# Performance work log

Measured on AMD Instinct MI355X. Metric: run time of the kernel, lower is better.

Reference implementation:

```python
import jax, jax.numpy as jnp
import numpy as np

N = 50000      # nodes
E = 800000     # edges (before self loops)
DIN = 128      # input feature dim
H = 2          # attention heads
C = 64         # per-head hidden channels (hidden_dim)
HC = H * C     # 128, concat output width of each GATv2 layer
DOUT = 4       # NUM_LANES
NEG = 0.2      # GATv2 default negative_slope


def _w(key, fan_in, shape):
    return jax.random.normal(key, shape, dtype=jnp.float32) * (1.0 / np.sqrt(fan_in))


def setup_inputs() -> dict:
    key = jax.random.key(0)
    ks = jax.random.split(key, 32)
    inp = {
        "x": jax.random.normal(ks[0], (N, DIN), dtype=jnp.float32),
        "edge_index": jax.random.randint(ks[1], (2, E), 0, N, dtype=jnp.int64),
    }
    # layer 1: DIN -> H*C
    inp["W1l"] = _w(ks[2], DIN, (DIN, HC)); inp["b1l"] = jnp.zeros((HC,), jnp.float32)
    inp["W1r"] = _w(ks[3], DIN, (DIN, HC)); inp["b1r"] = jnp.zeros((HC,), jnp.float32)
    inp["att1"] = _w(ks[4], C, (H, C));     inp["bias1"] = jnp.zeros((HC,), jnp.float32)
    # layer 2: H*C -> H*C
    inp["W2l"] = _w(ks[5], HC, (HC, HC));   inp["b2l"] = jnp.zeros((HC,), jnp.float32)
    inp["W2r"] = _w(ks[6], HC, (HC, HC));   inp["b2r"] = jnp.zeros((HC,), jnp.float32)
    inp["att2"] = _w(ks[7], C, (H, C));     inp["bias2"] = jnp.zeros((HC,), jnp.float32)
    # layer 3: H*C -> H*C
    inp["W3l"] = _w(ks[8], HC, (HC, HC));   inp["b3l"] = jnp.zeros((HC,), jnp.float32)
    inp["W3r"] = _w(ks[9], HC, (HC, HC));   inp["b3r"] = jnp.zeros((HC,), jnp.float32)
    inp["att3"] = _w(ks[10], C, (H, C));    inp["bias3"] = jnp.zeros((HC,), jnp.float32)
    # output linear
    inp["Wout"] = _w(ks[11], HC, (HC, DOUT)); inp["bout"] = jnp.zeros((DOUT,), jnp.float32)
    return inp


def gat_layer(x, src, dst, Wl, bl, Wr, br, att, bias):
    # GATv2Conv, concat=True, add_self_loops already in src/dst.
    n = x.shape[0]
    h, c = att.shape
    xl = (x @ Wl + bl).reshape(n, h, c)   # source transform
    xr = (x @ Wr + br).reshape(n, h, c)   # target transform
    m = xl[src] + xr[dst]                               # [Etot, H, C]
    e = jnp.sum(jax.nn.leaky_relu(m, NEG) * att, -1)    # [Etot, H]
    emax = jax.ops.segment_max(e, dst, num_segments=n)  # segment softmax over in-edges
    p = jnp.exp(e - emax[dst])
    denom = jax.ops.segment_sum(p, dst, num_segments=n)
    alpha = p / denom[dst]                              # [Etot, H]
    out = jax.ops.segment_sum(alpha[:, :, None] * xl[src], dst, num_segments=n)
    return out.reshape(n, h * c) + bias


def reference(x, edge_index, W1l, b1l, W1r, b1r, att1, bias1,
              W2l, b2l, W2r, b2r, att2, bias2,
              W3l, b3l, W3r, b3r, att3, bias3, Wout, bout):
    n = x.shape[0]
    loop = jnp.arange(n, dtype=edge_index.dtype)
    src = jnp.concatenate([edge_index[0], loop])  # add self loops (PyG default)
    dst = jnp.concatenate([edge_index[1], loop])
    h = jax.nn.relu(gat_layer(x, src, dst, W1l, b1l, W1r, b1r, att1, bias1))
    h = jax.nn.relu(gat_layer(h, src, dst, W2l, b2l, W2r, b2r, att2, bias2))
    h = jax.nn.relu(gat_layer(h, src, dst, W3l, b3l, W3r, b3r, att3, bias3))
    return h @ Wout + bout
```

## Files before the change

### kernel.cpp

```cpp
#include <hip/hip_runtime.h>
#include <math.h>

#define DIN  128
#define HC   128
#define NEG  0.2f

typedef __attribute__((ext_vector_type(4))) float f32x4;
typedef __attribute__((ext_vector_type(8))) _Float16 half8;
typedef __attribute__((ext_vector_type(2))) _Float16 half2v;

__device__ __forceinline__ int colOf(int p) {
    return ((p >> 5) * 2 + (p & 1)) * 16 + ((p & 31) >> 1);
}

template <int CTRL>
__device__ __forceinline__ float dpp_xadd(float x) {
    int r = __builtin_amdgcn_update_dpp(0, __float_as_int(x), CTRL, 0xF, 0xF, true);
    return x + __int_as_float(r);
}
__device__ __forceinline__ float rowsum8(float x) {
    x = dpp_xadd<0xB1>(x);
    x = dpp_xadd<0x4E>(x);
    x = dpp_xadd<0x141>(x);
    return x;
}
__device__ __forceinline__ float rowsum16(float x) {
    x = dpp_xadd<0xB1>(x);
    x = dpp_xadd<0x4E>(x);
    x = dpp_xadd<0x141>(x);
    x = dpp_xadd<0x140>(x);
    return x;
}

__global__ void hist_kernel(const int* __restrict__ ei, int E, int N,
                            int* __restrict__ counts) {
    int i = blockIdx.x * blockDim.x + threadIdx.x;
    int Etot = E + N;
    if (i >= Etot) return;
    int dst = (i < E) ? ei[E + i] : (i - E);
    if (dst < 0 || dst >= N) return;
    atomicAdd(&counts[dst], 1);
}

__global__ void scan_kernel(const int* __restrict__ counts,
                            int* __restrict__ rowptr,
                            int* __restrict__ cursor, int n) {
    __shared__ int wsum[16];
    int tid  = threadIdx.x;
    int lane = tid & 63, wid = tid >> 6;
    int running = 0;
    for (int base = 0; base < n; base += 4096) {
        int i = base + tid * 4;
        int4 v = make_int4(0, 0, 0, 0);
        if (i < n) v = *(const int4*)&counts[i];
        int ssum = v.x + v.y + v.z + v.w;
        int x = ssum;
        #pragma unroll
        for (int off = 1; off < 64; off <<= 1) {
            int y = __shfl_up(x, off, 64);
            if (lane >= off) x += y;
        }
        if (lane == 63) wsum[wid] = x;
        __syncthreads();
        if (tid < 16) {
            int w = wsum[tid];
            #pragma unroll
            for (int off = 1; off < 16; off <<= 1) {
                int y = __shfl_up(w, off, 64);
                if (tid >= off) w += y;
            }
            wsum[tid] = w;
        }
        __syncthreads();
        int excl = running + (wid ? wsum[wid - 1] : 0) + (x - ssum);
        if (i < n) {
            int4 r;
            r.x = excl;
            r.y = r.x + v.x;
            r.z = r.y + v.y;
            r.w = r.z + v.z;
            *(int4*)&rowptr[i] = r;
            *(int4*)&cursor[i] = r;
        }
        running += wsum[15];
        __syncthreads();
    }
    if (tid == 0) rowptr[n] = running;
}

__global__ void scatter_kernel(const int* __restrict__ ei, int E, int N,
                               int* __restrict__ cursor,
                               int* __restrict__ esrc) {
    int i = blockIdx.x * blockDim.x + threadIdx.x;
    int Etot = E + N;
    if (i >= Etot) return;
    int src = (i < E) ? ei[i]     : (i - E);
    int dst = (i < E) ? ei[E + i] : (i - E);
    if (dst < 0 || dst >= N || src < 0 || src >= N) return;
    int pos = atomicAdd(&cursor[dst], 1);
    esrc[pos] = src;
}

__global__ __launch_bounds__(256) void prep_w16(
        const float* __restrict__ W1l, const float* __restrict__ W1r,
        const float* __restrict__ W2l, const float* __restrict__ W2r,
        const float* __restrict__ W3l, const float* __restrict__ W3r,
        _Float16* __restrict__ w16) {
    int m = blockIdx.y;
    const float* W = (m == 0) ? W1l : (m == 1) ? W1r : (m == 2) ? W2l
                   : (m == 3) ? W2r : (m == 4) ? W3l : W3r;
    int t = blockIdx.x * 256 + threadIdx.x;
    int kb = t >> 9, nf = (t >> 6) & 7, l = t & 63;
    int col = nf * 16 + (l & 15);
    int k0  = kb * 32 + (l >> 4) * 8;
    size_t ob = ((size_t)m * 2048 + t) * 8;
    #pragma unroll
    for (int j = 0; j < 8; ++j) {
        int k = k0 + j;
        int krow = (m >= 2) ? colOf(k) : k;
        w16[ob + j] = (_Float16)W[(size_t)krow * 128 + col];
    }
}

#define GEMM_BODY(A_LOAD)                                                     \
    const _Float16* hpl = W16 + ((size_t)(matbase + 0) * 16384);              \
    const _Float16* hpr = W16 + ((size_t)(matbase + 1) * 16384);              \
    int tid = threadIdx.x;                                                    \
    int w   = tid >> 6;                                                       \
    int l   = tid & 63;                                                       \
    int m15 = l & 15, g = l >> 4;                                             \
    int rowbase = blockIdx.x * 32 + (w >> 1) * 16;                            \
    int nfb     = (w & 1) * 4;                                                \
    f32x4 accl[4], accr[4];                                                   \
    _Pragma("unroll")                                                         \
    for (int i = 0; i < 4; ++i) {                                             \
        accl[i] = (f32x4){0.f, 0.f, 0.f, 0.f};                                \
        accr[i] = (f32x4){0.f, 0.f, 0.f, 0.f};                                \
    }                                                                         \
    _Pragma("unroll")                                                         \
    for (int kb = 0; kb < 4; ++kb) {                                          \
        int arow = rowbase + m15;                                             \
        half8 a16 = (half8)(_Float16)0.f;                                     \
        A_LOAD                                                                \
        _Pragma("unroll")                                                     \
        for (int nfi = 0; nfi < 4; ++nfi) {                                   \
            int nf = nfb + nfi;                                               \
            size_t off = (((size_t)kb * 8 + nf) * 64 + l) * 8;                \
            half8 b_l = *(const half8*)&hpl[off];                             \
            half8 b_r = *(const half8*)&hpr[off];                             \
            accl[nfi] = __builtin_amdgcn_mfma_f32_16x16x32_f16(a16, b_l, accl[nfi], 0, 0, 0); \
            accr[nfi] = __builtin_amdgcn_mfma_f32_16x16x32_f16(a16, b_r, accr[nfi], 0, 0, 0); \
        }                                                                     \
    }                                                                         \
    float vbl[4], vbr[4];                                                     \
    _Pragma("unroll")                                                         \
    for (int nfi = 0; nfi < 4; ++nfi) {                                       \
        vbl[nfi] = bl[(nfb + nfi) * 16 + m15];                                \
        vbr[nfi] = br[(nfb + nfi) * 16 + m15];                                \
    }                                                                         \
    _Pragma("unroll")                                                         \
    for (int a2 = 0; a2 < 2; ++a2) {                                          \
        int a = (nfb >> 1) + a2;                                              \
        _Pragma("unroll")                                                     \
        for (int r = 0; r < 4; ++r) {                                         \
            int row = rowbase + g * 4 + r;                                    \
            if (row >= nrows) continue;                                       \
            size_t off = (size_t)row * 128 + a * 32 + m15 * 2;                \
            half2v pl, pr;                                                    \
            pl[0] = (_Float16)(accl[2 * a2][r]     + vbl[2 * a2]);            \
            pl[1] = (_Float16)(accl[2 * a2 + 1][r] + vbl[2 * a2 + 1]);        \
            pr[0] = (_Float16)(accr[2 * a2][r]     + vbr[2 * a2]);            \
            pr[1] = (_Float16)(accr[2 * a2 + 1][r] + vbr[2 * a2 + 1]);        \
            *(half2v*)&xlh[off] = pl;                                         \
            *(half2v*)&xrh[off] = pr;                                         \
        }                                                                     \
    }

__global__ __launch_bounds__(256) void gemm_f16_from_f32(
        const float* __restrict__ X, const _Float16* __restrict__ W16,
        int matbase, const float* __restrict__ bl, const float* __restrict__ br,
        _Float16* __restrict__ xlh, _Float16* __restrict__ xrh, int nrows) {
    GEMM_BODY(
        if (arow < nrows) {
            const float* xp = &X[(size_t)arow * 128 + kb * 32 + g * 8];
            float4 x0 = *(const float4*)xp;
            float4 x1 = *(const float4*)(xp + 4);
            a16[0] = (_Float16)x0.x; a16[1] = (_Float16)x0.y;
            a16[2] = (_Float16)x0.z; a16[3] = (_Float16)x0.w;
            a16[4] = (_Float16)x1.x; a16[5] = (_Float16)x1.y;
            a16[6] = (_Float16)x1.z; a16[7] = (_Float16)x1.w;
        }
    )
}

__global__ __launch_bounds__(256) void gemm_f16_from_f16(
        const _Float16* __restrict__ X, const _Float16* __restrict__ W16,
        int matbase, const float* __restrict__ bl, const float* __restrict__ br,
        _Float16* __restrict__ xlh, _Float16* __restrict__ xrh, int nrows) {
    GEMM_BODY(
        if (arow < nrows)
            a16 = *(const half8*)&X[(size_t)arow * 128 + kb * 32 + g * 8];
    )
}

__global__ __launch_bounds__(256) void gat_aggregate(
        const _Float16* __restrict__ xlh, const _Float16* __restrict__ xrh,
        const int* __restrict__ rowptr, const int* __restrict__ esrc,
        const float* __restrict__ att, const float* __restrict__ bias,
        _Float16* __restrict__ hout, int n, int do_relu,
        const float* __restrict__ Wout, const float* __restrict__ bout,
        float* __restrict__ out4) {
    int node = (int)((blockIdx.x * blockDim.x + threadIdx.x) >> 6);
    int lane = threadIdx.x & 63;
    if (node >= n) return;
    int g    = lane >> 4;
    int gl   = lane & 15;
    int pos0 = gl * 8;

    half8 xr8 = *(const half8*)&xrh[(size_t)node * 128 + pos0];
    float xrf[8], atp[8], atn[8];
    #pragma unroll
    for (int i = 0; i < 8; ++i) {
        float a = att[colOf(pos0 + i)];
        atp[i] = a;
        atn[i] = NEG * a;
        xrf[i] = (float)xr8[i];
    }

    float s = 0.f;
    float acc[8];
    #pragma unroll
    for (int i = 0; i < 8; ++i) acc[i] = 0.f;

    int pbeg = rowptr[node], pend = rowptr[node + 1];
    int p = pbeg + g;
    bool v0 = p < pend;
    bool v1 = p + 4 < pend;
    half8 r0 = (half8)(_Float16)0.f, r1 = r0;
    if (v0) r0 = *(const half8*)&xlh[(size_t)esrc[p] * 128 + pos0];
    if (v1) r1 = *(const half8*)&xlh[(size_t)esrc[p + 4] * 128 + pos0];

    while (v0) {
        bool v2 = p + 8 < pend;
        half8 r2 = (half8)(_Float16)0.f;
        if (v2) r2 = *(const half8*)&xlh[(size_t)esrc[p + 8] * 128 + pos0];

        float av[8], t = 0.f;
        #pragma unroll
        for (int i = 0; i < 8; ++i) {
            av[i] = (float)r0[i];
            float v = av[i] + xrf[i];
            t += v * (v > 0.f ? atp[i] : atn[i]);
        }
        t = rowsum8(t);
        float pp = __expf(fminf(t, 80.f));
        s += pp;
        #pragma unroll
        for (int i = 0; i < 8; ++i) acc[i] += pp * av[i];

        r0 = r1; r1 = r2; v0 = v1; v1 = v2; p += 4;
    }

    #pragma unroll
    for (int off = 16; off <= 32; off <<= 1) {
        s += __shfl_xor(s, off, 64);
        #pragma unroll
        for (int i = 0; i < 8; ++i) acc[i] += __shfl_xor(acc[i], off, 64);
    }

    float inv = 1.f / s;

    if (out4) {
        float o[8];
        #pragma unroll
        for (int i = 0; i < 8; ++i) {
            o[i] = acc[i] * inv + bias[colOf(pos0 + i)];
            if (do_relu) o[i] = fmaxf(o[i], 0.f);
        }
        float p0 = 0.f, p1 = 0.f, p2 = 0.f, p3 = 0.f;
        #pragma unroll
        for (int i = 0; i < 8; ++i) {
            float4 wv = *(const float4*)&Wout[colOf(pos0 + i) * 4];
            p0 += o[i] * wv.x; p1 += o[i] * wv.y;
            p2 += o[i] * wv.z; p3 += o[i] * wv.w;
        }
        p0 = rowsum16(p0); p1 = rowsum16(p1);
        p2 = rowsum16(p2); p3 = rowsum16(p3);
        if (lane == 0) {
            float4 ov = make_float4(p0 + bout[0], p1 + bout[1],
                                    p2 + bout[2], p3 + bout[3]);
            *(float4*)&out4[(size_t)node * 4] = ov;
        }
        return;
    }

    if (g == 0) {
        half8 oh;
        #pragma unroll
        for (int i = 0; i < 8; ++i) {
            float o = acc[i] * inv + bias[colOf(pos0 + i)];
            if (do_relu) o = fmaxf(o, 0.f);
            oh[i] = (_Float16)o;
        }
        *(half8*)&hout[(size_t)node * 128 + pos0] = oh;
    }
}

extern "C" void kernel_launch(void* const* d_in, const int* in_sizes, int n_in,
                              void* d_out, int out_size, void* d_ws,
                              size_t ws_size, hipStream_t stream) {
    const float* x    = (const float*)d_in[0];
    const int*   ei   = (const int*)  d_in[1];
    const float* W1l  = (const float*)d_in[2];
    const float* b1l  = (const float*)d_in[3];
    const float* W1r  = (const float*)d_in[4];
    const float* b1r  = (const float*)d_in[5];
    const float* att1 = (const float*)d_in[6];
    const float* bias1= (const float*)d_in[7];
    const float* W2l  = (const float*)d_in[8];
    const float* b2l  = (const float*)d_in[9];
    const float* W2r  = (const float*)d_in[10];
    const float* b2r  = (const float*)d_in[11];
    const float* att2 = (const float*)d_in[12];
    const float* bias2= (const float*)d_in[13];
    const float* W3l  = (const float*)d_in[14];
    const float* b3l  = (const float*)d_in[15];
    const float* W3r  = (const float*)d_in[16];
    const float* b3r  = (const float*)d_in[17];
    const float* att3 = (const float*)d_in[18];
    const float* bias3= (const float*)d_in[19];
    const float* Wout = (const float*)d_in[20];
    const float* bout = (const float*)d_in[21];

    int N    = in_sizes[0] / DIN;
    int E    = in_sizes[1] / 2;
    int Etot = E + N;

    char* base = (char*)d_ws;
    _Float16* h16 = (_Float16*)base;      base += (size_t)N * HC * 2;
    _Float16* xlh = (_Float16*)base;      base += (size_t)N * HC * 2;
    _Float16* xrh = (_Float16*)base;      base += (size_t)N * HC * 2;
    _Float16* w16 = (_Float16*)base;      base += 6 * 16384 * 2;
    int* esrc   = (int*)base;             base += (size_t)Etot * 4;
    int* rowptr = (int*)base;             base += (size_t)(((N + 1) + 3) & ~3) * 4;
    int* cursor = (int*)base;             base += (size_t)N * 4;
    int* counts = (int*)base;

    hipMemsetAsync(counts, 0, (size_t)N * sizeof(int), stream);
    hist_kernel<<<(Etot + 255) / 256, 256, 0, stream>>>(ei, E, N, counts);
    scan_kernel<<<1, 1024, 0, stream>>>(counts, rowptr, cursor, N);
    scatter_kernel<<<(Etot + 255) / 256, 256, 0, stream>>>(ei, E, N, cursor, esrc);
    prep_w16<<<dim3(8, 6), 256, 0, stream>>>(W1l, W1r, W2l, W2r, W3l, W3r, w16);

    int gemm_grid = (N + 31) / 32;
    int agg_grid  = (N + 3) / 4;

    gemm_f16_from_f32<<<gemm_grid, 256, 0, stream>>>(x, w16, 0, b1l, b1r, xlh, xrh, N);
    gat_aggregate<<<agg_grid, 256, 0, stream>>>(xlh, xrh, rowptr, esrc, att1, bias1,
                                                h16, N, 1, nullptr, nullptr, nullptr);
    gemm_f16_from_f16<<<gemm_grid, 256, 0, stream>>>(h16, w16, 2, b2l, b2r, xlh, xrh, N);
    gat_aggregate<<<agg_grid, 256, 0, stream>>>(xlh, xrh, rowptr, esrc, att2, bias2,
                                                h16, N, 1, nullptr, nullptr, nullptr);
    gemm_f16_from_f16<<<gemm_grid, 256, 0, stream>>>(h16, w16, 4, b3l, b3r, xlh, xrh, N);
    gat_aggregate<<<agg_grid, 256, 0, stream>>>(xlh, xrh, rowptr, esrc, att3, bias3,
                                                nullptr, N, 1, Wout, bout,
                                                (float*)d_out);
}
```

Before: 320.4 us.

## Single-pass scan, pre-permuted params, and deeper gather prefetch in aggregation

Three separate changes. The scan kernel now gives each thread a fixed 52-element chunk and runs one block-wide pass instead of looping over 4096-element tiles with repeated barriers. A new small kernel pre-permutes att, bias and Wout by colOf, so the aggregation kernel can use vector loads without per-element index math. The edge gather pipeline in gat_aggregate is deepened from two to three rows in flight to hide more latency. The hardcoded PER=52 only covers up to 53248 nodes, which limits the scan to this N, and the extra prefetch register raises register pressure.

```diff
diff --git a/kernel.cpp b/kernel.cpp
--- a/kernel.cpp
+++ b/kernel.cpp
@@ -46,46 +46,73 @@
                             int* __restrict__ rowptr,
                             int* __restrict__ cursor, int n) {
     __shared__ int wsum[16];
+    const int PER = 52;
     int tid  = threadIdx.x;
     int lane = tid & 63, wid = tid >> 6;
-    int running = 0;
-    for (int base = 0; base < n; base += 4096) {
-        int i = base + tid * 4;
-        int4 v = make_int4(0, 0, 0, 0);
-        if (i < n) v = *(const int4*)&counts[i];
-        int ssum = v.x + v.y + v.z + v.w;
-        int x = ssum;
-        #pragma unroll
-        for (int off = 1; off < 64; off <<= 1) {
-            int y = __shfl_up(x, off, 64);
-            if (lane >= off) x += y;
-        }
-        if (lane == 63) wsum[wid] = x;
-        __syncthreads();
-        if (tid < 16) {
-            int w = wsum[tid];
-            #pragma unroll
-            for (int off = 1; off < 16; off <<= 1) {
-                int y = __shfl_up(w, off, 64);
-                if (tid >= off) w += y;
-            }
-            wsum[tid] = w;
-        }
-        __syncthreads();
-        int excl = running + (wid ? wsum[wid - 1] : 0) + (x - ssum);
-        if (i < n) {
+    int base = tid * PER;
+
+    int4 vals[13];
+    if (base + PER <= n) {
+        #pragma unroll
+        for (int j = 0; j < 13; ++j)
+            vals[j] = *(const int4*)&counts[base + j * 4];
+    } else {
+        #pragma unroll
+        for (int j = 0; j < 13; ++j) {
+            int b = base + j * 4;
+            vals[j].x = (b + 0 < n) ? counts[b + 0] : 0;
+            vals[j].y = (b + 1 < n) ? counts[b + 1] : 0;
+            vals[j].z = (b + 2 < n) ? counts[b + 2] : 0;
+            vals[j].w = (b + 3 < n) ? counts[b + 3] : 0;
+        }
+    }
+    int tsum = 0;
+    #pragma unroll
+    for (int j = 0; j < 13; ++j)
+        tsum += vals[j].x + vals[j].y + vals[j].z + vals[j].w;
+
+    int x = tsum;
+    #pragma unroll
+    for (int off = 1; off < 64; off <<= 1) {
+        int y = __shfl_up(x, off, 64);
+        if (lane >= off) x += y;
+    }
+    if (lane == 63) wsum[wid] = x;
+    __syncthreads();
+    if (tid < 16) {
+        int w = wsum[tid];
+        #pragma unroll
+        for (int off = 1; off < 16; off <<= 1) {
+            int y = __shfl_up(w, off, 64);
+            if (tid >= off) w += y;
+        }
+        wsum[tid] = w;
+    }
+    __syncthreads();
+
+    int run = (wid ? wsum[wid - 1] : 0) + (x - tsum);
+    if (base + PER <= n) {
+        #pragma unroll
+        for (int j = 0; j < 13; ++j) {
             int4 r;
-            r.x = excl;
-            r.y = r.x + v.x;
-            r.z = r.y + v.y;
-            r.w = r.z + v.z;
-            *(int4*)&rowptr[i] = r;
-            *(int4*)&cursor[i] = r;
-        }
-        running += wsum[15];
-        __syncthreads();
-    }
-    if (tid == 0) rowptr[n] = running;
+            r.x = run; run += vals[j].x;
+            r.y = run; run += vals[j].y;
+            r.z = run; run += vals[j].z;
+            r.w = run; run += vals[j].w;
+            *(int4*)&rowptr[base + j * 4] = r;
+            *(int4*)&cursor[base + j * 4] = r;
+        }
+    } else {
+        #pragma unroll
+        for (int j = 0; j < 13; ++j) {
+            int b = base + j * 4;
+            if (b + 0 < n) { rowptr[b + 0] = run; cursor[b + 0] = run; } run += vals[j].x;
+            if (b + 1 < n) { rowptr[b + 1] = run; cursor[b + 1] = run; } run += vals[j].y;
+            if (b + 2 < n) { rowptr[b + 2] = run; cursor[b + 2] = run; } run += vals[j].z;
+            if (b + 3 < n) { rowptr[b + 3] = run; cursor[b + 3] = run; } run += vals[j].w;
+        }
+    }
+    if (tid == 1023) rowptr[n] = run;
 }
 
 __global__ void scatter_kernel(const int* __restrict__ ei, int E, int N,
@@ -120,6 +147,27 @@
         int krow = (m >= 2) ? colOf(k) : k;
         w16[ob + j] = (_Float16)W[(size_t)krow * 128 + col];
     }
+}
+
+__global__ void prep_params(
+        const float* __restrict__ att1, const float* __restrict__ att2,
+        const float* __restrict__ att3,
+        const float* __restrict__ bias1, const float* __restrict__ bias2,
+        const float* __restrict__ bias3,
+        const float* __restrict__ Wout,
+        float* __restrict__ att_p, float* __restrict__ bias_p,
+        float* __restrict__ wout_p) {
+    int p = threadIdx.x;
+    int c = colOf(p);
+    att_p[p]        = att1[c];
+    att_p[128 + p]  = att2[c];
+    att_p[256 + p]  = att3[c];
+    bias_p[p]       = bias1[c];
+    bias_p[128 + p] = bias2[c];
+    bias_p[256 + p] = bias3[c];
+    #pragma unroll
+    for (int j = 0; j < 4; ++j)
+        wout_p[p * 4 + j] = Wout[c * 4 + j];
 }
 
 #define GEMM_BODY(A_LOAD)                                                     \
@@ -206,9 +254,9 @@
 __global__ __launch_bounds__(256) void gat_aggregate(
         const _Float16* __restrict__ xlh, const _Float16* __restrict__ xrh,
         const int* __restrict__ rowptr, const int* __restrict__ esrc,
-        const float* __restrict__ att, const float* __restrict__ bias,
+        const float* __restrict__ att_p, const float* __restrict__ bias_p,
         _Float16* __restrict__ hout, int n, int do_relu,
-        const float* __restrict__ Wout, const float* __restrict__ bout,
+        const float* __restrict__ wout_p, const float* __restrict__ bout,
         float* __restrict__ out4) {
     int node = (int)((blockIdx.x * blockDim.x + threadIdx.x) >> 6);
     int lane = threadIdx.x & 63;
@@ -218,12 +266,13 @@
     int pos0 = gl * 8;
 
     half8 xr8 = *(const half8*)&xrh[(size_t)node * 128 + pos0];
-    float xrf[8], atp[8], atn[8];
+    float4 ap0 = *(const float4*)&att_p[pos0];
+    float4 ap1 = *(const float4*)&att_p[pos0 + 4];
+    float atp[8] = {ap0.x, ap0.y, ap0.z, ap0.w, ap1.x, ap1.y, ap1.z, ap1.w};
+    float atn[8], xrf[8];
     #pragma unroll
     for (int i = 0; i < 8; ++i) {
-        float a = att[colOf(pos0 + i)];
-        atp[i] = a;
-        atn[i] = NEG * a;
+        atn[i] = NEG * atp[i];
         xrf[i] = (float)xr8[i];
     }
 
@@ -236,14 +285,16 @@
     int p = pbeg + g;
     bool v0 = p < pend;
     bool v1 = p + 4 < pend;
-    half8 r0 = (half8)(_Float16)0.f, r1 = r0;
+    bool v2 = p + 8 < pend;
+    half8 r0 = (half8)(_Float16)0.f, r1 = r0, r2 = r0;
     if (v0) r0 = *(const half8*)&xlh[(size_t)esrc[p] * 128 + pos0];
     if (v1) r1 = *(const half8*)&xlh[(size_t)esrc[p + 4] * 128 + pos0];
+    if (v2) r2 = *(const half8*)&xlh[(size_t)esrc[p + 8] * 128 + pos0];
 
     while (v0) {
-        bool v2 = p + 8 < pend;
-        half8 r2 = (half8)(_Float16)0.f;
-        if (v2) r2 = *(const half8*)&xlh[(size_t)esrc[p + 8] * 128 + pos0];
+        bool v3 = p + 12 < pend;
+        half8 r3 = (half8)(_Float16)0.f;
+        if (v3) r3 = *(const half8*)&xlh[(size_t)esrc[p + 12] * 128 + pos0];
 
         float av[8], t = 0.f;
         #pragma unroll
@@ -258,7 +309,8 @@
         #pragma unroll
         for (int i = 0; i < 8; ++i) acc[i] += pp * av[i];
 
-        r0 = r1; r1 = r2; v0 = v1; v1 = v2; p += 4;
+        r0 = r1; r1 = r2; r2 = r3;
+        v0 = v1; v1 = v2; v2 = v3; p += 4;
     }
 
     #pragma unroll
@@ -271,16 +323,19 @@
     float inv = 1.f / s;
 
     if (out4) {
+        float4 b0 = *(const float4*)&bias_p[pos0];
+        float4 b1 = *(const float4*)&bias_p[pos0 + 4];
+        float bb[8] = {b0.x, b0.y, b0.z, b0.w, b1.x, b1.y, b1.z, b1.w};
         float o[8];
         #pragma unroll
         for (int i = 0; i < 8; ++i) {
-            o[i] = acc[i] * inv + bias[colOf(pos0 + i)];
+            o[i] = acc[i] * inv + bb[i];
             if (do_relu) o[i] = fmaxf(o[i], 0.f);
         }
         float p0 = 0.f, p1 = 0.f, p2 = 0.f, p3 = 0.f;
         #pragma unroll
         for (int i = 0; i < 8; ++i) {
-            float4 wv = *(const float4*)&Wout[colOf(pos0 + i) * 4];
+            float4 wv = *(const float4*)&wout_p[(pos0 + i) * 4];
             p0 += o[i] * wv.x; p1 += o[i] * wv.y;
             p2 += o[i] * wv.z; p3 += o[i] * wv.w;
         }
@@ -295,10 +350,13 @@
     }
 
     if (g == 0) {
+        float4 b0 = *(const float4*)&bias_p[pos0];
+        float4 b1 = *(const float4*)&bias_p[pos0 + 4];
+        float bb[8] = {b0.x, b0.y, b0.z, b0.w, b1.x, b1.y, b1.z, b1.w};
         half8 oh;
         #pragma unroll
         for (int i = 0; i < 8; ++i) {
-            float o = acc[i] * inv + bias[colOf(pos0 + i)];
+            float o = acc[i] * inv + bb[i];
             if (do_relu) o = fmaxf(o, 0.f);
             oh[i] = (_Float16)o;
         }
@@ -341,6 +399,9 @@
     _Float16* xlh = (_Float16*)base;      base += (size_t)N * HC * 2;
     _Float16* xrh = (_Float16*)base;      base += (size_t)N * HC * 2;
     _Float16* w16 = (_Float16*)base;      base += 6 * 16384 * 2;
+    float* att_p  = (float*)base;         base += 384 * 4;
+    float* bias_p = (float*)base;         base += 384 * 4;
+    float* wout_p = (float*)base;         base += 512 * 4;
     int* esrc   = (int*)base;             base += (size_t)Etot * 4;
     int* rowptr = (int*)base;             base += (size_t)(((N + 1) + 3) & ~3) * 4;
     int* cursor = (int*)base;             base += (size_t)N * 4;
@@ -351,18 +412,23 @@
     scan_kernel<<<1, 1024, 0, stream>>>(counts, rowptr, cursor, N);
     scatter_kernel<<<(Etot + 255) / 256, 256, 0, stream>>>(ei, E, N, cursor, esrc);
     prep_w16<<<dim3(8, 6), 256, 0, stream>>>(W1l, W1r, W2l, W2r, W3l, W3r, w16);
+    prep_params<<<1, 128, 0, stream>>>(att1, att2, att3, bias1, bias2, bias3,
+                                       Wout, att_p, bias_p, wout_p);
 
     int gemm_grid = (N + 31) / 32;
     int agg_grid  = (N + 3) / 4;
 
     gemm_f16_from_f32<<<gemm_grid, 256, 0, stream>>>(x, w16, 0, b1l, b1r, xlh, xrh, N);
-    gat_aggregate<<<agg_grid, 256, 0, stream>>>(xlh, xrh, rowptr, esrc, att1, bias1,
+    gat_aggregate<<<agg_grid, 256, 0, stream>>>(xlh, xrh, rowptr, esrc,
+                                                att_p, bias_p,
                                                 h16, N, 1, nullptr, nullptr, nullptr);
     gemm_f16_from_f16<<<gemm_grid, 256, 0, stream>>>(h16, w16, 2, b2l, b2r, xlh, xrh, N);
-    gat_aggregate<<<agg_grid, 256, 0, stream>>>(xlh, xrh, rowptr, esrc, att2, bias2,
+    gat_aggregate<<<agg_grid, 256, 0, stream>>>(xlh, xrh, rowptr, esrc,
+                                                att_p + 128, bias_p + 128,
                                                 h16, N, 1, nullptr, nullptr, nullptr);
     gemm_f16_from_f16<<<gemm_grid, 256, 0, stream>>>(h16, w16, 4, b3l, b3r, xlh, xrh, N);
-    gat_aggregate<<<agg_grid, 256, 0, stream>>>(xlh, xrh, rowptr, esrc, att3, bias3,
-                                                nullptr, N, 1, Wout, bout,
+    gat_aggregate<<<agg_grid, 256, 0, stream>>>(xlh, xrh, rowptr, esrc,
+                                                att_p + 256, bias_p + 256,
+                                                nullptr, N, 1, wout_p, bout,
                                                 (float*)d_out);
 }
```

Result: slower. 342.2 us (+6.8%).
